# Performance work log

Hardware: AMD Instinct MI355X
Metric: run time of the kernel (lower is better)

Reference implementation:

```python
import jax, jax.numpy as jnp
import numpy as np

N = 100000
E = 3200000
IN_C = 128
HID = 128


def setup_inputs() -> dict:
    key = jax.random.key(0)
    k1, k2, k3, k4, k5 = jax.random.split(key, 5)
    x = jax.random.normal(k1, (N, IN_C), dtype=jnp.float32)
    edge_index = jax.random.randint(k2, (2, E), 0, N, dtype=jnp.int64)
    edge_weight = jax.random.uniform(k3, (E,), dtype=jnp.float32)
    # GCNConv linear weight [out, in] (applied as x @ W.T), glorot-ish scale
    W = jax.random.normal(k4, (HID, IN_C), dtype=jnp.float32) / np.sqrt(IN_C)
    bias = jnp.zeros((HID,), dtype=jnp.float32)
    # PReLU per-channel alpha, torch default init 0.25
    alpha = jnp.full((HID,), 0.25, dtype=jnp.float32)
    return {"x": x, "edge_index": edge_index, "edge_weight": edge_weight,
            "W": W, "bias": bias, "alpha": alpha}


def reference(x, edge_index, edge_weight, W, bias, alpha):
    n = x.shape[0]
    # gcn_norm with self-loops (fill value 1.0)
    loop_idx = jnp.arange(n, dtype=edge_index.dtype)
    row = jnp.concatenate([edge_index[0], loop_idx])  # source
    col = jnp.concatenate([edge_index[1], loop_idx])  # target
    ew = jnp.concatenate([edge_weight, jnp.ones((n,), dtype=edge_weight.dtype)])
    deg = jax.ops.segment_sum(ew, col, num_segments=n)  # in-degree by weight
    dinv = jnp.where(deg > 0, jax.lax.rsqrt(deg), 0.0)
    norm = dinv[row] * ew * dinv[col]  # [E+N]
    # linear transform first (GCNConv order), then gather-scatter aggregation
    h = x @ W.T  # [N, HID]
    msgs = norm[:, None] * h[row]  # [E+N, HID]
    out = jax.ops.segment_sum(msgs, col, num_segments=n) + bias  # [N, HID]
    # PReLU with per-channel alpha
    return jnp.where(out > 0, out, alpha * out)
```

## Files before the change

kernel.cpp:

```cpp
#include <hip/hip_runtime.h>


#define NBLK    512
#define MAXBKT  1600
#define QSCALE  32767.0f
#define SBS     16

typedef float vfloat2 __attribute__((ext_vector_type(2)));

__device__ __forceinline__ unsigned bf16pack2(float a, float b) {
    unsigned ua = __float_as_uint(a);
    ua = (ua + 0x7fffu + ((ua >> 16) & 1u)) >> 16;
    unsigned ub = __float_as_uint(b);
    ub = (ub + 0x7fffu + ((ub >> 16) & 1u)) >> 16;
    return ua | (ub << 16);
}

__device__ __forceinline__ float2 bf16unpack2(unsigned u) {
    return make_float2(__uint_as_float(u << 16),
                       __uint_as_float(u & 0xffff0000u));
}

__global__ __launch_bounds__(256) void p1_hist(const int* __restrict__ col,
                                               unsigned* __restrict__ hist,
                                               int e, int nbkt, int epb) {
    __shared__ unsigned lh[MAXBKT];
    int b = blockIdx.x;
    for (int k = threadIdx.x; k < nbkt; k += 256) lh[k] = 0;
    __syncthreads();
    int s = b * epb, en = s + epb; if (en > e) en = e;
    for (int i = s + threadIdx.x; i < en; i += 256)
        atomicAdd(&lh[col[i] >> 6], 1u);
    __syncthreads();
    for (int k = threadIdx.x; k < nbkt; k += 256)
        hist[(size_t)k * NBLK + b] = lh[k];
}

__global__ __launch_bounds__(1024) void scan_partial2(
    const unsigned* __restrict__ a, unsigned* __restrict__ part, int m) {
    __shared__ unsigned red[1024];
    int t = threadIdx.x, i = blockIdx.x * 1024 + t;
    red[t] = (i < m) ? a[i] : 0;
    __syncthreads();
    #pragma unroll
    for (int d = 512; d > 0; d >>= 1) {
        if (t < d) red[t] += red[t + d];
        __syncthreads();
    }
    if (t == 0) part[blockIdx.x] = red[0];
}

__global__ __launch_bounds__(1024) void scan_base2(
    unsigned* __restrict__ part, int nb, int* __restrict__ offs, int n, int e) {
    __shared__ unsigned s[1024];
    int t = threadIdx.x;
    unsigned v = (t < nb) ? part[t] : 0;
    s[t] = v;
    __syncthreads();
    for (int d = 1; d < 1024; d <<= 1) {
        unsigned add = (t >= d) ? s[t - d] : 0;
        __syncthreads();
        s[t] += add;
        __syncthreads();
    }
    if (t < nb) part[t] = s[t] - v;
    if (t == 0) offs[n] = e;
}

__global__ __launch_bounds__(1024) void scan_write2(
    unsigned* __restrict__ a, const unsigned* __restrict__ part, int m) {
    __shared__ unsigned s[1024];
    int t = threadIdx.x, i = blockIdx.x * 1024 + t;
    unsigned v = (i < m) ? a[i] : 0;
    s[t] = v;
    __syncthreads();
    for (int d = 1; d < 1024; d <<= 1) {
        unsigned add = (t >= d) ? s[t - d] : 0;
        __syncthreads();
        s[t] += add;
        __syncthreads();
    }
    if (i < m) a[i] = part[blockIdx.x] + s[t] - v;
}

__global__ __launch_bounds__(256) void p2_scatter(
    const int* __restrict__ col, const int* __restrict__ row,
    const float* __restrict__ ew, const unsigned* __restrict__ base,
    unsigned long long* __restrict__ pay, int e, int nbkt, int epb) {
    __shared__ unsigned lbase[MAXBKT];
    __shared__ unsigned lcur[MAXBKT];
    int b = blockIdx.x;
    for (int k = threadIdx.x; k < nbkt; k += 256) {
        lbase[k] = base[(size_t)k * NBLK + b];
        lcur[k] = 0;
    }
    __syncthreads();
    int s = b * epb, en = s + epb; if (en > e) en = e;
    for (int i = s + threadIdx.x; i < en; i += 256) {
        int c = col[i];
        int bk = c >> 6;
        unsigned q  = (unsigned)(ew[i] * QSCALE + 0.5f);
        unsigned lo = ((unsigned)row[i] << 15) | q;
        unsigned rk = atomicAdd(&lcur[bk], 1u);
        pay[(size_t)lbase[bk] + rk] =
            ((unsigned long long)(unsigned)(c & 63) << 32) | lo;
    }
}

__global__ __launch_bounds__(256) void p3_build(
    const unsigned long long* __restrict__ pay,
    const unsigned* __restrict__ histBase,
    unsigned* __restrict__ csr, int* __restrict__ offs,
    float* __restrict__ dinv, int n, int nbkt, int e) {
    __shared__ unsigned cnt[64][SBS], lofs[64][SBS], cur[64][SBS];
    __shared__ unsigned wsum[64], tbase[64], ttot[64];
    int bk = blockIdx.x;
    int zs = (int)histBase[(size_t)bk * NBLK];
    int ze = (bk + 1 < nbkt) ? (int)histBase[(size_t)(bk + 1) * NBLK] : e;
    int t = threadIdx.x;
    for (int k = t; k < 64 * SBS; k += 256) {
        (&cnt[0][0])[k] = 0;
        (&cur[0][0])[k] = 0;
    }
    if (t < 64) wsum[t] = 0;
    __syncthreads();
    for (int p = zs + t; p < ze; p += 256) {
        unsigned long long v = pay[p];
        int l = (int)(v >> 32) & 63;
        unsigned lo = (unsigned)v;
        int sb = (int)((lo >> 15) >> 13);
        atomicAdd(&cnt[l][sb], 1u);
        atomicAdd(&wsum[l], lo & 0x7fffu);
    }
    __syncthreads();
    if (t < 64) {
        unsigned s = 0;
        #pragma unroll
        for (int j = 0; j < SBS; ++j) s += cnt[t][j];
        ttot[t] = s;
    }
    __syncthreads();
    if (t == 0) {
        unsigned run = 0;
        for (int l = 0; l < 64; ++l) { tbase[l] = run; run += ttot[l]; }
    }
    __syncthreads();
    if (t < 64) {
        unsigned run = tbase[t];
        #pragma unroll
        for (int j = 0; j < SBS; ++j) { lofs[t][j] = run; run += cnt[t][j]; }
    }
    __syncthreads();
    for (int p = zs + t; p < ze; p += 256) {
        unsigned long long v = pay[p];
        int l = (int)(v >> 32) & 63;
        unsigned lo = (unsigned)v;
        int sb = (int)((lo >> 15) >> 13);
        unsigned rk = atomicAdd(&cur[l][sb], 1u);
        csr[zs + lofs[l][sb] + rk] = lo;
    }
    if (t < 64) {
        int node = bk * 64 + t;
        if (node < n) {
            offs[node] = zs + (int)tbase[t];
            float dg = 1.0f + (float)wsum[t] * (1.0f / QSCALE);
            dinv[node] = rsqrtf(dg);
        }
    }
}

__global__ __launch_bounds__(256) void csr2_fill(const unsigned* __restrict__ csr,
                                                 const float* __restrict__ dinv,
                                                 unsigned* __restrict__ csr2, int e) {
    int i = blockIdx.x * 256 + threadIdx.x;
    if (i < e) {
        unsigned v = csr[i];
        float a = dinv[v >> 15] * ((float)(v & 0x7fffu) * (1.0f / QSCALE));
        csr2[i] = (v & 0xffff8000u) | (unsigned)(a * QSCALE + 0.5f);
    }
}

__global__ __launch_bounds__(256) void gemm_kernel(const float* __restrict__ x,
                                                   const float* __restrict__ W,
                                                   unsigned* __restrict__ h, int n) {
    __shared__ float Wt[128][128];
    int t = threadIdx.x;
    const float4* W4 = (const float4*)W;
    #pragma unroll
    for (int it = 0; it < 16; ++it) {
        int i = t + it * 256;
        float4 v = W4[i];
        int o  = i >> 5;
        int kb = (i & 31) << 2;
        Wt[kb + 0][o ^ (((kb + 0) & 7) << 2)] = v.x;
        Wt[kb + 1][o ^ (((kb + 1) & 7) << 2)] = v.y;
        Wt[kb + 2][o ^ (((kb + 2) & 7) << 2)] = v.z;
        Wt[kb + 3][o ^ (((kb + 3) & 7) << 2)] = v.w;
    }
    __syncthreads();

    int tc = t & 31;
    int rs = t >> 5;
    int r0 = blockIdx.x * 64 + rs * 8;
    if (r0 >= n) return;
    const float4* x4 = (const float4*)x;

    float acc[8][4];
    #pragma unroll
    for (int ri = 0; ri < 8; ++ri)
        #pragma unroll
        for (int j = 0; j < 4; ++j) acc[ri][j] = 0.0f;

    int rcnt = n - r0; if (rcnt > 8) rcnt = 8;

    if (rcnt == 8) {
        for (int kq = 0; kq < 32; ++kq) {
            int kb = kq << 2;
            float4 wv0 = *(const float4*)&Wt[kb + 0][(4 * tc) ^ (((kb + 0) & 7) << 2)];
            float4 wv1 = *(const float4*)&Wt[kb + 1][(4 * tc) ^ (((kb + 1) & 7) << 2)];
            float4 wv2 = *(const float4*)&Wt[kb + 2][(4 * tc) ^ (((kb + 2) & 7) << 2)];
            float4 wv3 = *(const float4*)&Wt[kb + 3][(4 * tc) ^ (((kb + 3) & 7) << 2)];
            #pragma unroll
            for (int ri = 0; ri < 8; ++ri) {
                float4 xv = x4[(size_t)(r0 + ri) * 32 + kq];
                acc[ri][0] += xv.x * wv0.x + xv.y * wv1.x + xv.z * wv2.x + xv.w * wv3.x;
                acc[ri][1] += xv.x * wv0.y + xv.y * wv1.y + xv.z * wv2.y + xv.w * wv3.y;
                acc[ri][2] += xv.x * wv0.z + xv.y * wv1.z + xv.z * wv2.z + xv.w * wv3.z;
                acc[ri][3] += xv.x * wv0.w + xv.y * wv1.w + xv.z * wv2.w + xv.w * wv3.w;
            }
        }
        uint2* h2 = (uint2*)h;
        #pragma unroll
        for (int ri = 0; ri < 8; ++ri)
            h2[(size_t)(r0 + ri) * 32 + tc] =
                make_uint2(bf16pack2(acc[ri][0], acc[ri][1]),
                           bf16pack2(acc[ri][2], acc[ri][3]));
    } else {
        for (int kq = 0; kq < 32; ++kq) {
            int kb = kq << 2;
            float4 wv0 = *(const float4*)&Wt[kb + 0][(4 * tc) ^ (((kb + 0) & 7) << 2)];
            float4 wv1 = *(const float4*)&Wt[kb + 1][(4 * tc) ^ (((kb + 1) & 7) << 2)];
            float4 wv2 = *(const float4*)&Wt[kb + 2][(4 * tc) ^ (((kb + 2) & 7) << 2)];
            float4 wv3 = *(const float4*)&Wt[kb + 3][(4 * tc) ^ (((kb + 3) & 7) << 2)];
            for (int ri = 0; ri < rcnt; ++ri) {
                float4 xv = x4[(size_t)(r0 + ri) * 32 + kq];
                acc[ri][0] += xv.x * wv0.x + xv.y * wv1.x + xv.z * wv2.x + xv.w * wv3.x;
                acc[ri][1] += xv.x * wv0.y + xv.y * wv1.y + xv.z * wv2.y + xv.w * wv3.y;
                acc[ri][2] += xv.x * wv0.z + xv.y * wv1.z + xv.z * wv2.z + xv.w * wv3.z;
                acc[ri][3] += xv.x * wv0.w + xv.y * wv1.w + xv.z * wv2.w + xv.w * wv3.w;
            }
        }
        uint2* h2 = (uint2*)h;
        for (int ri = 0; ri < rcnt; ++ri)
            h2[(size_t)(r0 + ri) * 32 + tc] =
                make_uint2(bf16pack2(acc[ri][0], acc[ri][1]),
                           bf16pack2(acc[ri][2], acc[ri][3]));
    }
}

__global__ __launch_bounds__(256) void aggregate_kernel(
    const unsigned* __restrict__ h, const unsigned* __restrict__ csr2,
    const int* __restrict__ offs, const float* __restrict__ dinv,
    const float* __restrict__ bias, const float* __restrict__ alpha,
    float* __restrict__ out, int n, int swzq) {
    int bid = blockIdx.x;
    int sb  = swzq ? ((bid & 7) * swzq + (bid >> 3)) : bid;
    int w = sb * 4 + (threadIdx.x >> 6);
    if (w >= n) return;
    int lane = threadIdx.x & 63;

    int beg = __builtin_amdgcn_readfirstlane(offs[w]);
    int end = __builtin_amdgcn_readfirstlane(offs[w + 1]);
    float ax = 0.0f, ay = 0.0f;

    int i = beg;
    int end4 = beg + ((end - beg) & ~3);
    for (; i < end4; i += 4) {
        unsigned v0 = __builtin_nontemporal_load(&csr2[i]);
        unsigned v1 = __builtin_nontemporal_load(&csr2[i + 1]);
        unsigned v2 = __builtin_nontemporal_load(&csr2[i + 2]);
        unsigned v3 = __builtin_nontemporal_load(&csr2[i + 3]);
        unsigned u0 = h[(size_t)(v0 >> 15) * 64 + lane];
        unsigned u1 = h[(size_t)(v1 >> 15) * 64 + lane];
        unsigned u2 = h[(size_t)(v2 >> 15) * 64 + lane];
        unsigned u3 = h[(size_t)(v3 >> 15) * 64 + lane];
        float a0 = (float)(v0 & 0x7fffu) * (1.0f / QSCALE);
        float a1 = (float)(v1 & 0x7fffu) * (1.0f / QSCALE);
        float a2 = (float)(v2 & 0x7fffu) * (1.0f / QSCALE);
        float a3 = (float)(v3 & 0x7fffu) * (1.0f / QSCALE);
        float2 h0 = bf16unpack2(u0), h1 = bf16unpack2(u1);
        float2 h2 = bf16unpack2(u2), h3 = bf16unpack2(u3);
        ax += a0 * h0.x; ay += a0 * h0.y;
        ax += a1 * h1.x; ay += a1 * h1.y;
        ax += a2 * h2.x; ay += a2 * h2.y;
        ax += a3 * h3.x; ay += a3 * h3.y;
    }
    for (; i < end; ++i) {
        unsigned v = __builtin_nontemporal_load(&csr2[i]);
        unsigned u = h[(size_t)(v >> 15) * 64 + lane];
        float a = (float)(v & 0x7fffu) * (1.0f / QSCALE);
        float2 hv = bf16unpack2(u);
        ax += a * hv.x; ay += a * hv.y;
    }

    float dc = dinv[w];
    float2 hc = bf16unpack2(h[(size_t)w * 64 + lane]);
    ax += dc * hc.x; ay += dc * hc.y;

    float2 bv = ((const float2*)bias)[lane];
    float2 av = ((const float2*)alpha)[lane];
    float ox = ax * dc + bv.x;
    float oy = ay * dc + bv.y;
    ox = ox > 0.0f ? ox : av.x * ox;
    oy = oy > 0.0f ? oy : av.y * oy;
    vfloat2 ov; ov.x = ox; ov.y = oy;
    __builtin_nontemporal_store(ov,
        (vfloat2*)&((float2*)out)[(size_t)w * 64 + lane]);
}

extern "C" void kernel_launch(void* const* d_in, const int* in_sizes, int n_in,
                              void* d_out, int out_size, void* d_ws, size_t ws_size,
                              hipStream_t stream) {
    const float* x     = (const float*)d_in[0];
    const int*   ei    = (const int*)d_in[1];
    const float* ew    = (const float*)d_in[2];
    const float* W     = (const float*)d_in[3];
    const float* bias  = (const float*)d_in[4];
    const float* alpha = (const float*)d_in[5];
    float* out = (float*)d_out;

    const int n = in_sizes[0] / 128;
    const int e = in_sizes[1] / 2;
    const int* row = ei;
    const int* col = ei + e;

    const int nbkt = (n + 63) >> 6;
    const int m    = nbkt * NBLK;
    const int epb  = (e + NBLK - 1) / NBLK;
    const int nb2  = (m + 1023) / 1024;

    char* ws = (char*)d_ws;
    size_t off = 0;
    auto alloc = [&](size_t bytes) -> char* {
        char* p = ws + off;
        off = (off + bytes + 255) & ~(size_t)255;
        return p;
    };
    unsigned*           hist = (unsigned*)          alloc((size_t)m * 4);
    unsigned*           part = (unsigned*)          alloc((size_t)1024 * 4);
    int*                offs = (int*)               alloc((size_t)(n + 1) * 4);
    float*              dinv = (float*)             alloc((size_t)n * 4);
    unsigned long long* pay  = (unsigned long long*)alloc((size_t)e * 8);
    unsigned*           csr  = (unsigned*)          alloc((size_t)e * 4);
    unsigned*           csr2 = (unsigned*)          alloc((size_t)e * 4);
    unsigned*           h    = (unsigned*)          alloc((size_t)n * 128 * 2);
    (void)ws_size; (void)n_in; (void)out_size;

    p1_hist<<<NBLK, 256, 0, stream>>>(col, hist, e, nbkt, epb);
    scan_partial2<<<nb2, 1024, 0, stream>>>(hist, part, m);
    scan_base2<<<1, 1024, 0, stream>>>(part, nb2, offs, n, e);
    scan_write2<<<nb2, 1024, 0, stream>>>(hist, part, m);
    p2_scatter<<<NBLK, 256, 0, stream>>>(col, row, ew, hist, pay, e, nbkt, epb);
    p3_build<<<nbkt, 256, 0, stream>>>(pay, hist, csr, offs, dinv, n, nbkt, e);
    csr2_fill<<<(e + 255) / 256, 256, 0, stream>>>(csr, dinv, csr2, e);

    int gg = (n + 63) / 64;
    gemm_kernel<<<gg, 256, 0, stream>>>(x, W, h, n);

    int ga = (n + 3) / 4;
    int swzq = (ga % 8 == 0) ? ga / 8 : 0;
    aggregate_kernel<<<ga, 256, 0, stream>>>(h, csr2, offs, dinv,
                                             bias, alpha, out, n, swzq);
}
```

Before: 294.4 us.

## Fuse edge scatter with GEMM and pack scatter payload into 32 bits

Merges the bucket-scatter pass and the dense x@W.T GEMM into one launch, with block-index dispatch, so the latency-bound scatter overlaps with compute-bound GEMM blocks. It also shrinks the scatter payload from 64 to 32 bits by quantising edge weights to 9 bits (the local column takes 6 bits and the source row 17), which halves pay traffic in the scatter and build passes. The cost is coarser edge-weight precision in the degree and norm computation, and a 17-bit source field that only covers up to about 131k nodes. The fused kernel now uses 64KB of shared memory for every block, including the scatter blocks, which may lower occupancy for that part.

```diff
diff --git a/kernel.cpp b/kernel.cpp
--- a/kernel.cpp
+++ b/kernel.cpp
@@ -4,6 +4,7 @@
 #define NBLK    512
 #define MAXBKT  1600
 #define QSCALE  32767.0f
+#define Q9      511.0f
 #define SBS     16
 
 typedef float vfloat2 __attribute__((ext_vector_type(2)));
@@ -83,108 +84,38 @@
     if (i < m) a[i] = part[blockIdx.x] + s[t] - v;
 }
 
-__global__ __launch_bounds__(256) void p2_scatter(
+__global__ __launch_bounds__(256) void fused_p2_gemm(
     const int* __restrict__ col, const int* __restrict__ row,
     const float* __restrict__ ew, const unsigned* __restrict__ base,
-    unsigned long long* __restrict__ pay, int e, int nbkt, int epb) {
-    __shared__ unsigned lbase[MAXBKT];
-    __shared__ unsigned lcur[MAXBKT];
-    int b = blockIdx.x;
-    for (int k = threadIdx.x; k < nbkt; k += 256) {
-        lbase[k] = base[(size_t)k * NBLK + b];
-        lcur[k] = 0;
-    }
-    __syncthreads();
-    int s = b * epb, en = s + epb; if (en > e) en = e;
-    for (int i = s + threadIdx.x; i < en; i += 256) {
-        int c = col[i];
-        int bk = c >> 6;
-        unsigned q  = (unsigned)(ew[i] * QSCALE + 0.5f);
-        unsigned lo = ((unsigned)row[i] << 15) | q;
-        unsigned rk = atomicAdd(&lcur[bk], 1u);
-        pay[(size_t)lbase[bk] + rk] =
-            ((unsigned long long)(unsigned)(c & 63) << 32) | lo;
-    }
-}
-
-__global__ __launch_bounds__(256) void p3_build(
-    const unsigned long long* __restrict__ pay,
-    const unsigned* __restrict__ histBase,
-    unsigned* __restrict__ csr, int* __restrict__ offs,
-    float* __restrict__ dinv, int n, int nbkt, int e) {
-    __shared__ unsigned cnt[64][SBS], lofs[64][SBS], cur[64][SBS];
-    __shared__ unsigned wsum[64], tbase[64], ttot[64];
-    int bk = blockIdx.x;
-    int zs = (int)histBase[(size_t)bk * NBLK];
-    int ze = (bk + 1 < nbkt) ? (int)histBase[(size_t)(bk + 1) * NBLK] : e;
+    unsigned* __restrict__ pay, int e, int nbkt, int epb,
+    const float* __restrict__ x, const float* __restrict__ W,
+    unsigned* __restrict__ h, int n) {
+    __shared__ float smem[128 * 128];
+    int bid = blockIdx.x;
     int t = threadIdx.x;
-    for (int k = t; k < 64 * SBS; k += 256) {
-        (&cnt[0][0])[k] = 0;
-        (&cur[0][0])[k] = 0;
-    }
-    if (t < 64) wsum[t] = 0;
-    __syncthreads();
-    for (int p = zs + t; p < ze; p += 256) {
-        unsigned long long v = pay[p];
-        int l = (int)(v >> 32) & 63;
-        unsigned lo = (unsigned)v;
-        int sb = (int)((lo >> 15) >> 13);
-        atomicAdd(&cnt[l][sb], 1u);
-        atomicAdd(&wsum[l], lo & 0x7fffu);
-    }
-    __syncthreads();
-    if (t < 64) {
-        unsigned s = 0;
-        #pragma unroll
-        for (int j = 0; j < SBS; ++j) s += cnt[t][j];
-        ttot[t] = s;
-    }
-    __syncthreads();
-    if (t == 0) {
-        unsigned run = 0;
-        for (int l = 0; l < 64; ++l) { tbase[l] = run; run += ttot[l]; }
-    }
-    __syncthreads();
-    if (t < 64) {
-        unsigned run = tbase[t];
-        #pragma unroll
-        for (int j = 0; j < SBS; ++j) { lofs[t][j] = run; run += cnt[t][j]; }
-    }
-    __syncthreads();
-    for (int p = zs + t; p < ze; p += 256) {
-        unsigned long long v = pay[p];
-        int l = (int)(v >> 32) & 63;
-        unsigned lo = (unsigned)v;
-        int sb = (int)((lo >> 15) >> 13);
-        unsigned rk = atomicAdd(&cur[l][sb], 1u);
-        csr[zs + lofs[l][sb] + rk] = lo;
-    }
-    if (t < 64) {
-        int node = bk * 64 + t;
-        if (node < n) {
-            offs[node] = zs + (int)tbase[t];
-            float dg = 1.0f + (float)wsum[t] * (1.0f / QSCALE);
-            dinv[node] = rsqrtf(dg);
-        }
-    }
-}
-
-__global__ __launch_bounds__(256) void csr2_fill(const unsigned* __restrict__ csr,
-                                                 const float* __restrict__ dinv,
-                                                 unsigned* __restrict__ csr2, int e) {
-    int i = blockIdx.x * 256 + threadIdx.x;
-    if (i < e) {
-        unsigned v = csr[i];
-        float a = dinv[v >> 15] * ((float)(v & 0x7fffu) * (1.0f / QSCALE));
-        csr2[i] = (v & 0xffff8000u) | (unsigned)(a * QSCALE + 0.5f);
-    }
-}
-
-__global__ __launch_bounds__(256) void gemm_kernel(const float* __restrict__ x,
-                                                   const float* __restrict__ W,
-                                                   unsigned* __restrict__ h, int n) {
-    __shared__ float Wt[128][128];
-    int t = threadIdx.x;
+
+    if (bid < NBLK) {
+        unsigned* lbase = (unsigned*)smem;
+        unsigned* lcur  = (unsigned*)smem + MAXBKT;
+        int b = bid;
+        for (int k = t; k < nbkt; k += 256) {
+            lbase[k] = base[(size_t)k * NBLK + b];
+            lcur[k] = 0;
+        }
+        __syncthreads();
+        int s = b * epb, en = s + epb; if (en > e) en = e;
+        for (int i = s + t; i < en; i += 256) {
+            int c = col[i];
+            int bk = c >> 6;
+            unsigned q = (unsigned)(ew[i] * Q9 + 0.5f);
+            unsigned rk = atomicAdd(&lcur[bk], 1u);
+            pay[(size_t)lbase[bk] + rk] =
+                ((unsigned)(c & 63) << 26) | ((unsigned)row[i] << 9) | q;
+        }
+        return;
+    }
+
+    float (*Wt)[128] = (float (*)[128])smem;
     const float4* W4 = (const float4*)W;
     #pragma unroll
     for (int it = 0; it < 16; ++it) {
@@ -201,7 +132,7 @@
 
     int tc = t & 31;
     int rs = t >> 5;
-    int r0 = blockIdx.x * 64 + rs * 8;
+    int r0 = (bid - NBLK) * 64 + rs * 8;
     if (r0 >= n) return;
     const float4* x4 = (const float4*)x;
 
@@ -255,6 +186,79 @@
             h2[(size_t)(r0 + ri) * 32 + tc] =
                 make_uint2(bf16pack2(acc[ri][0], acc[ri][1]),
                            bf16pack2(acc[ri][2], acc[ri][3]));
+    }
+}
+
+__global__ __launch_bounds__(256) void p3_build(
+    const unsigned* __restrict__ pay,
+    const unsigned* __restrict__ histBase,
+    unsigned* __restrict__ csr, int* __restrict__ offs,
+    float* __restrict__ dinv, int n, int nbkt, int e) {
+    __shared__ unsigned cnt[64][SBS], lofs[64][SBS], cur[64][SBS];
+    __shared__ unsigned wsum[64], tbase[64], ttot[64];
+    int bk = blockIdx.x;
+    int zs = (int)histBase[(size_t)bk * NBLK];
+    int ze = (bk + 1 < nbkt) ? (int)histBase[(size_t)(bk + 1) * NBLK] : e;
+    int t = threadIdx.x;
+    for (int k = t; k < 64 * SBS; k += 256) {
+        (&cnt[0][0])[k] = 0;
+        (&cur[0][0])[k] = 0;
+    }
+    if (t < 64) wsum[t] = 0;
+    __syncthreads();
+    for (int p = zs + t; p < ze; p += 256) {
+        unsigned v = pay[p];
+        int l = (int)(v >> 26);
+        int sb = (int)(((v >> 9) & 0x1ffffu) >> 13);
+        atomicAdd(&cnt[l][sb], 1u);
+        atomicAdd(&wsum[l], v & 0x1ffu);
+    }
+    __syncthreads();
+    if (t < 64) {
+        unsigned s = 0;
+        #pragma unroll
+        for (int j = 0; j < SBS; ++j) s += cnt[t][j];
+        ttot[t] = s;
+    }
+    __syncthreads();
+    if (t == 0) {
+        unsigned run = 0;
+        for (int l = 0; l < 64; ++l) { tbase[l] = run; run += ttot[l]; }
+    }
+    __syncthreads();
+    if (t < 64) {
+        unsigned run = tbase[t];
+        #pragma unroll
+        for (int j = 0; j < SBS; ++j) { lofs[t][j] = run; run += cnt[t][j]; }
+    }
+    __syncthreads();
+    for (int p = zs + t; p < ze; p += 256) {
+        unsigned v = pay[p];
+        int l = (int)(v >> 26);
+        unsigned lo = v & 0x03ffffffu;
+        int sb = (int)((lo >> 9) >> 13);
+        unsigned rk = atomicAdd(&cur[l][sb], 1u);
+        csr[zs + lofs[l][sb] + rk] = lo;
+    }
+    if (t < 64) {
+        int node = bk * 64 + t;
+        if (node < n) {
+            offs[node] = zs + (int)tbase[t];
+            float dg = 1.0f + (float)wsum[t] * (1.0f / Q9);
+            dinv[node] = rsqrtf(dg);
+        }
+    }
+}
+
+__global__ __launch_bounds__(256) void csr2_fill(const unsigned* __restrict__ csr,
+                                                 const float* __restrict__ dinv,
+                                                 unsigned* __restrict__ csr2, int e) {
+    int i = blockIdx.x * 256 + threadIdx.x;
+    if (i < e) {
+        unsigned v = csr[i];
+        unsigned src = v >> 9;
+        float a = dinv[src] * ((float)(v & 0x1ffu) * (1.0f / Q9));
+        csr2[i] = (src << 15) | (unsigned)(a * QSCALE + 0.5f);
     }
 }
 
@@ -346,26 +350,26 @@
         off = (off + bytes + 255) & ~(size_t)255;
         return p;
     };
-    unsigned*           hist = (unsigned*)          alloc((size_t)m * 4);
-    unsigned*           part = (unsigned*)          alloc((size_t)1024 * 4);
-    int*                offs = (int*)               alloc((size_t)(n + 1) * 4);
-    float*              dinv = (float*)             alloc((size_t)n * 4);
-    unsigned long long* pay  = (unsigned long long*)alloc((size_t)e * 8);
-    unsigned*           csr  = (unsigned*)          alloc((size_t)e * 4);
-    unsigned*           csr2 = (unsigned*)          alloc((size_t)e * 4);
-    unsigned*           h    = (unsigned*)          alloc((size_t)n * 128 * 2);
+    unsigned* hist = (unsigned*)alloc((size_t)m * 4);
+    unsigned* part = (unsigned*)alloc((size_t)1024 * 4);
+    int*      offs = (int*)     alloc((size_t)(n + 1) * 4);
+    float*    dinv = (float*)   alloc((size_t)n * 4);
+    unsigned* pay  = (unsigned*)alloc((size_t)e * 4);
+    unsigned* csr  = (unsigned*)alloc((size_t)e * 4);
+    unsigned* csr2 = (unsigned*)alloc((size_t)e * 4);
+    unsigned* h    = (unsigned*)alloc((size_t)n * 128 * 2);
     (void)ws_size; (void)n_in; (void)out_size;
+
+    int gg = (n + 63) / 64;
 
     p1_hist<<<NBLK, 256, 0, stream>>>(col, hist, e, nbkt, epb);
     scan_partial2<<<nb2, 1024, 0, stream>>>(hist, part, m);
     scan_base2<<<1, 1024, 0, stream>>>(part, nb2, offs, n, e);
     scan_write2<<<nb2, 1024, 0, stream>>>(hist, part, m);
-    p2_scatter<<<NBLK, 256, 0, stream>>>(col, row, ew, hist, pay, e, nbkt, epb);
+    fused_p2_gemm<<<NBLK + gg, 256, 0, stream>>>(col, row, ew, hist, pay,
+                                                 e, nbkt, epb, x, W, h, n);
     p3_build<<<nbkt, 256, 0, stream>>>(pay, hist, csr, offs, dinv, n, nbkt, e);
     csr2_fill<<<(e + 255) / 256, 256, 0, stream>>>(csr, dinv, csr2, e);
-
-    int gg = (n + 63) / 64;
-    gemm_kernel<<<gg, 256, 0, stream>>>(x, W, h, n);
 
     int ga = (n + 3) / 4;
     int swzq = (ga % 8 == 0) ? ga / 8 : 0;
```

Result: faster. 288.1 us (-2.1%).
